# Kernel optimization log

Measured on AMD Instinct MI355X. Metric: run time of the kernel, lower is better.

Reference implementation:

```python
import jax, jax.numpy as jnp
import numpy as np

B, L, DM, H, PD = 2, 1024, 512, 8, 64
D = DM // H  # head_dim = 64
NEG = -10000.0


def setup_inputs() -> dict:
    key = jax.random.key(0)
    ks = jax.random.split(key, 12)
    s = 1.0 / np.sqrt(DM)
    sp = 1.0 / np.sqrt(PD)
    return {
        "x": jax.random.normal(ks[0], (B, L, DM), dtype=jnp.float32),
        "z": jax.random.normal(ks[1], (B, L, L, PD), dtype=jnp.float32),
        "residue_mask": jnp.ones((B, L), dtype=bool),
        "Wq": jax.random.normal(ks[2], (DM, DM), dtype=jnp.float32) * s,
        "bq": jnp.zeros((DM,), dtype=jnp.float32),
        "Wk": jax.random.normal(ks[3], (DM, DM), dtype=jnp.float32) * s,
        "bk": jnp.zeros((DM,), dtype=jnp.float32),
        "Wv": jax.random.normal(ks[4], (DM, DM), dtype=jnp.float32) * s,
        "bv": jnp.zeros((DM,), dtype=jnp.float32),
        "Wo": jax.random.normal(ks[5], (DM, DM), dtype=jnp.float32) * s,
        "bo": jnp.zeros((DM,), dtype=jnp.float32),
        "Wpb": jax.random.normal(ks[6], (PD, H), dtype=jnp.float32) * sp,
    }


def reference(x, z, residue_mask, Wq, bq, Wk, bk, Wv, bv, Wo, bo, Wpb):
    b, l, c = x.shape
    scale = 1.0 / np.sqrt(D)
    # projections -> (B, H, L, D)
    q = (x @ Wq + bq).reshape(b, l, H, D).transpose(0, 2, 1, 3)
    k = (x @ Wk + bk).reshape(b, l, H, D).transpose(0, 2, 1, 3)
    v = (x @ Wv + bv).reshape(b, l, H, D).transpose(0, 2, 1, 3)
    # pair bias: (B, L, L, PD) @ (PD, H) -> (B, H, L, L)
    bias = jnp.einsum('bijp,ph->bhij', z, Wpb)
    logits = jnp.einsum('bhid,bhjd->bhij', q, k) * scale + bias
    key_ok = residue_mask[:, None, None, :]
    query_ok = residue_mask[:, None, :, None]
    logits = jnp.where(key_ok, logits, NEG)
    logits = jnp.where(query_ok, logits, NEG)
    attn = jax.nn.softmax(logits, axis=-1)
    out = jnp.einsum('bhij,bhjd->bhid', attn, v)
    out = out.transpose(0, 2, 1, 3).reshape(b, l, c)
    return out @ Wo + bo
```

## Files before the change

### kernel.cpp

```cpp
#include <hip/hip_runtime.h>

typedef __bf16 bf16;
typedef __attribute__((ext_vector_type(4))) __bf16 bf16x4;
typedef __attribute__((ext_vector_type(8))) __bf16 bf16x8;
typedef __attribute__((ext_vector_type(4))) float f32x4;
typedef __attribute__((ext_vector_type(4))) _Float16 f16x4;
typedef __attribute__((ext_vector_type(2))) _Float16 f16x2;

#define B_   2
#define L_   1024
#define DM_  512
#define H_   8
#define D_   64
#define PD_  64
#define NEG_VAL -10000.0f

#define XB_N   (2048*512)
#define WT_N   (1536*512)
#define WTO_N  (512*512)
#define WTPB_N (16*64)

static __device__ __forceinline__ f32x4 mfma_bf16(bf16x8 a, bf16x8 b, f32x4 c) {
  return __builtin_amdgcn_mfma_f32_16x16x32_bf16(a, b, c, 0, 0, 0);
}

__global__ __launch_bounds__(256) void prep_kernel(
    const float* __restrict__ x, const float* __restrict__ Wq, const float* __restrict__ Wk,
    const float* __restrict__ Wv, const float* __restrict__ Wo, const float* __restrict__ Wpb,
    bf16* __restrict__ xb, bf16* __restrict__ Wt, bf16* __restrict__ Wto, bf16* __restrict__ Wtpb) {
  const int total = XB_N + WT_N + WTO_N + WTPB_N;
  for (int idx = blockIdx.x * 256 + threadIdx.x; idx < total; idx += gridDim.x * 256) {
    if (idx < XB_N) {
      xb[idx] = (bf16)x[idx];
    } else if (idx < XB_N + WT_N) {
      int t = idx - XB_N;
      int n = t >> 9, kk = t & 511;
      int sel = n >> 9, nn = n & 511;
      const float* W = sel == 0 ? Wq : (sel == 1 ? Wk : Wv);
      Wt[t] = (bf16)W[kk * 512 + nn];
    } else if (idx < XB_N + WT_N + WTO_N) {
      int t = idx - XB_N - WT_N;
      int n = t >> 9, kk = t & 511;
      Wto[t] = (bf16)Wo[kk * 512 + n];
    } else {
      int t = idx - XB_N - WT_N - WTO_N;
      int n = t >> 6, kk = t & 63;
      Wtpb[t] = (n < 8) ? (bf16)Wpb[kk * 8 + n] : (bf16)0.0f;
    }
  }
}

__global__ __launch_bounds__(256) void qkv_gemm(
    const bf16* __restrict__ xb, const bf16* __restrict__ Wt,
    const float* __restrict__ bq, const float* __restrict__ bk, const float* __restrict__ bv,
    bf16* __restrict__ qb, bf16* __restrict__ kb, bf16* __restrict__ vT) {
  int wid = blockIdx.x * 4 + (threadIdx.x >> 6);
  int lane = threadIdx.x & 63;
  int mt = wid / 48, nt = wid - mt * 48;
  int row0 = mt * 32, col0 = nt * 32;
  int lr = lane & 15, lg = lane >> 4;
  const bf16* a0p = xb + (row0 + lr) * 512 + lg * 8;
  const bf16* a1p = a0p + 16 * 512;
  const bf16* b0p = Wt + (col0 + lr) * 512 + lg * 8;
  const bf16* b1p = b0p + 16 * 512;
  f32x4 acc00 = {0.f,0.f,0.f,0.f}, acc01 = acc00, acc10 = acc00, acc11 = acc00;
#pragma unroll
  for (int kk = 0; kk < 512; kk += 32) {
    bf16x8 a0 = *reinterpret_cast<const bf16x8*>(a0p + kk);
    bf16x8 a1 = *reinterpret_cast<const bf16x8*>(a1p + kk);
    bf16x8 b0 = *reinterpret_cast<const bf16x8*>(b0p + kk);
    bf16x8 b1 = *reinterpret_cast<const bf16x8*>(b1p + kk);
    acc00 = mfma_bf16(a0, b0, acc00);
    acc01 = mfma_bf16(a0, b1, acc01);
    acc10 = mfma_bf16(a1, b0, acc10);
    acc11 = mfma_bf16(a1, b1, acc11);
  }
#pragma unroll
  for (int ni = 0; ni < 2; ++ni) {
    int col = col0 + ni * 16 + lr;
    int wsel = col >> 9;
    int ncol = col & 511;
    int h = ncol >> 6, d = ncol & 63;
    const float* bias = wsel == 0 ? bq : (wsel == 1 ? bk : bv);
    float bval = bias[ncol];
#pragma unroll
    for (int mi = 0; mi < 2; ++mi) {
      f32x4 acc = (mi == 0) ? (ni == 0 ? acc00 : acc01) : (ni == 0 ? acc10 : acc11);
      int m0 = row0 + mi * 16 + lg * 4;
      int bidx = m0 >> 10, l0 = m0 & 1023;
      if (wsel == 2) {
        bf16x4 pv;
#pragma unroll
        for (int r = 0; r < 4; ++r) pv[r] = (bf16)(acc[r] + bval);
        *reinterpret_cast<bf16x4*>(vT + ((long)(bidx * H_ + h) * D_ + d) * L_ + l0) = pv;
      } else if (wsel == 0) {
#pragma unroll
        for (int r = 0; r < 4; ++r)
          qb[((long)(bidx * H_ + h) * L_ + l0 + r) * D_ + d] = (bf16)((acc[r] + bval) * 0.125f);
      } else {
#pragma unroll
        for (int r = 0; r < 4; ++r)
          kb[((long)(bidx * H_ + h) * L_ + l0 + r) * D_ + d] = (bf16)(acc[r] + bval);
      }
    }
  }
}

__global__ __launch_bounds__(256) void bias_gemm(
    const float* __restrict__ z, const bf16* __restrict__ Wtpb, _Float16* __restrict__ biasbuf) {
  __shared__ float zt_raw[64 * 64];
  __shared__ _Float16 bt[8][72];
  int tid = threadIdx.x;
  int w = tid >> 6, lane = tid & 63;
  int lr = lane & 15, lg = lane >> 4;
  char* zb = (char*)zt_raw;
  const char* zsrc = (const char*)(z + (long)blockIdx.x * 4096);
#pragma unroll
  for (int q = 0; q < 4; ++q) {
    int lb = q * 4096 + tid * 16;
    int row = lb >> 8, col = lb & 255;
    f32x4 v = *reinterpret_cast<const f32x4*>(zsrc + lb);
    *reinterpret_cast<f32x4*>(zb + row * 256 + (col ^ ((row & 7) << 5))) = v;
  }
  bf16x8 b0 = *reinterpret_cast<const bf16x8*>(Wtpb + lr * 64 + lg * 8);
  bf16x8 b1 = *reinterpret_cast<const bf16x8*>(Wtpb + lr * 64 + 32 + lg * 8);
  __syncthreads();
  int row = w * 16 + lr;
  int sw = (row & 7) << 5;
  const char* zr = zb + row * 256;
  f32x4 z0 = *reinterpret_cast<const f32x4*>(zr + ((lg * 32) ^ sw));
  f32x4 z1 = *reinterpret_cast<const f32x4*>(zr + (((lg * 32) ^ sw) + 16));
  f32x4 z2 = *reinterpret_cast<const f32x4*>(zr + ((128 + lg * 32) ^ sw));
  f32x4 z3 = *reinterpret_cast<const f32x4*>(zr + (((128 + lg * 32) ^ sw) + 16));
  bf16x8 a0, a1;
#pragma unroll
  for (int e = 0; e < 4; ++e) { a0[e] = (bf16)z0[e]; a0[e + 4] = (bf16)z1[e]; }
#pragma unroll
  for (int e = 0; e < 4; ++e) { a1[e] = (bf16)z2[e]; a1[e + 4] = (bf16)z3[e]; }
  f32x4 acc = {0.f, 0.f, 0.f, 0.f};
  acc = mfma_bf16(a0, b0, acc);
  acc = mfma_bf16(a1, b1, acc);
  __syncthreads();
  if (lr < 8) {
    f16x4 hv;
#pragma unroll
    for (int r = 0; r < 4; ++r) hv[r] = (_Float16)acc[r];
    *reinterpret_cast<f16x4*>(&bt[lr][w * 16 + lg * 4]) = hv;
  }
  __syncthreads();
  {
    int h = tid >> 5, part = tid & 31;
    long pb = (long)blockIdx.x * 64;
    int b = (int)(pb >> 20), i = ((int)(pb >> 10)) & 1023, j0 = (int)pb & 1023;
    _Float16* dst = biasbuf + ((((long)b * H_ + h) * L_ + i) << 10) + j0 + part * 2;
    *reinterpret_cast<f16x2*>(dst) = *reinterpret_cast<const f16x2*>(&bt[h][part * 2]);
  }
}

__global__ __launch_bounds__(256) void attn_kernel(
    const bf16* __restrict__ qb, const bf16* __restrict__ kb, const bf16* __restrict__ vT,
    const _Float16* __restrict__ biasbuf, const int* __restrict__ mask, bf16* __restrict__ attn_out) {
  __shared__ bf16  p_lds[4][16][64];
  __shared__ float o_lds[4][16][64];
  __shared__ float m_lds[4][16];
  __shared__ float l_lds[4][16];
  int bid = blockIdx.x;
  int b = bid >> 9, h = (bid >> 6) & 7, it = bid & 63;
  int i0 = it * 16;
  int tid = threadIdx.x, w = tid >> 6, lane = tid & 63, lr = lane & 15, lg = lane >> 4;

  const bf16* qrow = qb + ((long)(b * H_ + h) * L_ + i0 + lr) * D_ + lg * 8;
  bf16x8 qa0 = *reinterpret_cast<const bf16x8*>(qrow);
  bf16x8 qa1 = *reinterpret_cast<const bf16x8*>(qrow + 32);
  const bf16* kbase = kb + (long)(b * H_ + h) * L_ * D_;
  const bf16* vbase = vT + (long)(b * H_ + h) * D_ * L_;
  const _Float16* bias_base = biasbuf + ((long)(b * H_ + h) * L_ + i0) * L_;
  const int* mrow_mask = mask + b * L_;

  bool qok[4];
#pragma unroll
  for (int r = 0; r < 4; ++r) qok[r] = mrow_mask[i0 + lg * 4 + r] != 0;

  float mr[4] = {-3.0e38f, -3.0e38f, -3.0e38f, -3.0e38f};
  float lsum[4] = {0.f, 0.f, 0.f, 0.f};
  f32x4 o0 = {0.f,0.f,0.f,0.f}, o1 = o0, o2 = o0, o3 = o0;

  char* p_base = (char*)&p_lds[w][0][0];

  for (int jt = 0; jt < 4; ++jt) {
    int j0 = w * 256 + jt * 64;
    f32x4 s0, s1, s2, s3;
#pragma unroll
    for (int jsub = 0; jsub < 4; ++jsub) {
      int j = j0 + jsub * 16 + lr;
      f32x4 acc;
#pragma unroll
      for (int r = 0; r < 4; ++r) acc[r] = (float)bias_base[(long)(lg * 4 + r) * L_ + j];
      const bf16* kr = kbase + (long)j * D_ + lg * 8;
      acc = mfma_bf16(qa0, *reinterpret_cast<const bf16x8*>(kr), acc);
      acc = mfma_bf16(qa1, *reinterpret_cast<const bf16x8*>(kr + 32), acc);
      bool kok = mrow_mask[j] != 0;
      if (!kok) {
#pragma unroll
        for (int r = 0; r < 4; ++r) acc[r] = NEG_VAL;
      }
      if (jsub == 0) s0 = acc; else if (jsub == 1) s1 = acc; else if (jsub == 2) s2 = acc; else s3 = acc;
    }
#pragma unroll
    for (int r = 0; r < 4; ++r) {
      if (!qok[r]) { s0[r] = NEG_VAL; s1[r] = NEG_VAL; s2[r] = NEG_VAL; s3[r] = NEG_VAL; }
    }
#pragma unroll
    for (int r = 0; r < 4; ++r) {
      float mt_ = fmaxf(fmaxf(s0[r], s1[r]), fmaxf(s2[r], s3[r]));
#pragma unroll
      for (int off = 1; off <= 8; off <<= 1) mt_ = fmaxf(mt_, __shfl_xor(mt_, off));
      float mnew = fmaxf(mr[r], mt_);
      float alpha = __expf(mr[r] - mnew);
      mr[r] = mnew;
      float p0 = __expf(s0[r] - mnew);
      float p1 = __expf(s1[r] - mnew);
      float p2 = __expf(s2[r] - mnew);
      float p3 = __expf(s3[r] - mnew);
      float ps = p0 + p1 + p2 + p3;
#pragma unroll
      for (int off = 1; off <= 8; off <<= 1) ps += __shfl_xor(ps, off);
      lsum[r] = lsum[r] * alpha + ps;
      o0[r] *= alpha; o1[r] *= alpha; o2[r] *= alpha; o3[r] *= alpha;
      int row = lg * 4 + r;
      int sw = (row & 7) << 4;
      *(bf16*)(p_base + row * 128 + ((lr * 2) ^ sw)) = (bf16)p0;
      *(bf16*)(p_base + row * 128 + ((32 + lr * 2) ^ sw)) = (bf16)p1;
      *(bf16*)(p_base + row * 128 + ((64 + lr * 2) ^ sw)) = (bf16)p2;
      *(bf16*)(p_base + row * 128 + ((96 + lr * 2) ^ sw)) = (bf16)p3;
    }
    int swr = (lr & 7) << 4;
    bf16x8 pa0 = *(const bf16x8*)(p_base + lr * 128 + ((lg * 16) ^ swr));
    bf16x8 pa1 = *(const bf16x8*)(p_base + lr * 128 + ((64 + lg * 16) ^ swr));
#pragma unroll
    for (int dsub = 0; dsub < 4; ++dsub) {
      const bf16* vr = vbase + (long)(dsub * 16 + lr) * L_ + j0 + lg * 8;
      bf16x8 vb0 = *reinterpret_cast<const bf16x8*>(vr);
      bf16x8 vb1 = *reinterpret_cast<const bf16x8*>(vr + 32);
      f32x4 acc = (dsub == 0) ? o0 : (dsub == 1) ? o1 : (dsub == 2) ? o2 : o3;
      acc = mfma_bf16(pa0, vb0, acc);
      acc = mfma_bf16(pa1, vb1, acc);
      if (dsub == 0) o0 = acc; else if (dsub == 1) o1 = acc; else if (dsub == 2) o2 = acc; else o3 = acc;
    }
  }
#pragma unroll
  for (int r = 0; r < 4; ++r) {
    int row = lg * 4 + r;
    o_lds[w][row][0 * 16 + lr] = o0[r];
    o_lds[w][row][1 * 16 + lr] = o1[r];
    o_lds[w][row][2 * 16 + lr] = o2[r];
    o_lds[w][row][3 * 16 + lr] = o3[r];
    if (lr == 0) { m_lds[w][row] = mr[r]; l_lds[w][row] = lsum[r]; }
  }
  __syncthreads();
  {
    int row = tid >> 4, d0 = (tid & 15) * 4;
    float M = fmaxf(fmaxf(m_lds[0][row], m_lds[1][row]), fmaxf(m_lds[2][row], m_lds[3][row]));
    float lt = 0.f;
    float oacc[4] = {0.f, 0.f, 0.f, 0.f};
#pragma unroll
    for (int ww = 0; ww < 4; ++ww) {
      float c = __expf(m_lds[ww][row] - M);
      lt += c * l_lds[ww][row];
#pragma unroll
      for (int e = 0; e < 4; ++e) oacc[e] += c * o_lds[ww][row][d0 + e];
    }
    float inv = 1.0f / lt;
    bf16x4 ov;
#pragma unroll
    for (int e = 0; e < 4; ++e) ov[e] = (bf16)(oacc[e] * inv);
    *reinterpret_cast<bf16x4*>(attn_out + ((long)(b * L_ + i0 + row)) * DM_ + h * D_ + d0) = ov;
  }
}

__global__ __launch_bounds__(256) void out_gemm(
    const bf16* __restrict__ ab, const bf16* __restrict__ Wto,
    const float* __restrict__ bo, float* __restrict__ out) {
  int wid = blockIdx.x * 4 + (threadIdx.x >> 6);
  int lane = threadIdx.x & 63;
  int mt = wid >> 4, nt = wid & 15;
  int row0 = mt * 32, col0 = nt * 32;
  int lr = lane & 15, lg = lane >> 4;
  const bf16* a0p = ab + (row0 + lr) * 512 + lg * 8;
  const bf16* a1p = a0p + 16 * 512;
  const bf16* b0p = Wto + (col0 + lr) * 512 + lg * 8;
  const bf16* b1p = b0p + 16 * 512;
  f32x4 acc00 = {0.f,0.f,0.f,0.f}, acc01 = acc00, acc10 = acc00, acc11 = acc00;
#pragma unroll
  for (int kk = 0; kk < 512; kk += 32) {
    bf16x8 a0 = *reinterpret_cast<const bf16x8*>(a0p + kk);
    bf16x8 a1 = *reinterpret_cast<const bf16x8*>(a1p + kk);
    bf16x8 b0 = *reinterpret_cast<const bf16x8*>(b0p + kk);
    bf16x8 b1 = *reinterpret_cast<const bf16x8*>(b1p + kk);
    acc00 = mfma_bf16(a0, b0, acc00);
    acc01 = mfma_bf16(a0, b1, acc01);
    acc10 = mfma_bf16(a1, b0, acc10);
    acc11 = mfma_bf16(a1, b1, acc11);
  }
#pragma unroll
  for (int ni = 0; ni < 2; ++ni) {
    int col = col0 + ni * 16 + lr;
    float bval = bo[col];
#pragma unroll
    for (int mi = 0; mi < 2; ++mi) {
      f32x4 acc = (mi == 0) ? (ni == 0 ? acc00 : acc01) : (ni == 0 ? acc10 : acc11);
      int m0 = row0 + mi * 16 + lg * 4;
#pragma unroll
      for (int r = 0; r < 4; ++r) out[(long)(m0 + r) * 512 + col] = acc[r] + bval;
    }
  }
}

extern "C" void kernel_launch(void* const* d_in, const int* in_sizes, int n_in,
                              void* d_out, int out_size, void* d_ws, size_t ws_size,
                              hipStream_t stream) {
  const float* x    = (const float*)d_in[0];
  const float* z    = (const float*)d_in[1];
  const int*   mask = (const int*)d_in[2];
  const float* Wq   = (const float*)d_in[3];
  const float* bq   = (const float*)d_in[4];
  const float* Wk   = (const float*)d_in[5];
  const float* bk   = (const float*)d_in[6];
  const float* Wv   = (const float*)d_in[7];
  const float* bv   = (const float*)d_in[8];
  const float* Wo   = (const float*)d_in[9];
  const float* bo   = (const float*)d_in[10];
  const float* Wpb  = (const float*)d_in[11];

  char* ws = (char*)d_ws;
  bf16* xb        = (bf16*)(ws + 0);
  bf16* Wt        = (bf16*)(ws + 2097152);
  bf16* Wto       = (bf16*)(ws + 3670016);
  bf16* Wtpb      = (bf16*)(ws + 4194304);
  bf16* qbuf      = (bf16*)(ws + 4196352);
  bf16* kbuf      = (bf16*)(ws + 6293504);
  bf16* vTbuf     = (bf16*)(ws + 8390656);
  bf16* attn_out  = (bf16*)(ws + 10487808);
  _Float16* biasb = (_Float16*)(ws + 12584960);

  prep_kernel<<<2048, 256, 0, stream>>>(x, Wq, Wk, Wv, Wo, Wpb, xb, Wt, Wto, Wtpb);
  qkv_gemm<<<768, 256, 0, stream>>>(xb, Wt, bq, bk, bv, qbuf, kbuf, vTbuf);
  bias_gemm<<<32768, 256, 0, stream>>>(z, Wtpb, biasb);
  attn_kernel<<<1024, 256, 0, stream>>>(qbuf, kbuf, vTbuf, biasb, mask, attn_out);
  out_gemm<<<256, 256, 0, stream>>>(attn_out, Wto, bo, (float*)d_out);
}
```

Baseline: 194.6 us.

## Split attention keys across blocks with separate merge kernel; fold key mask into bias

The attention kernel is split into a partial kernel that processes half the keys per block (2048 blocks), writing per-wave partial O/m/l to global memory, followed by a merge8 kernel that combines 8 partials per row. The MFMA operands are swapped so each lane owns a query row, which turns the row reductions into two cross-lane shuffles and lets bias be loaded as vector f16x4. The key mask is applied in bias_gemm so it no longer has to be applied in the attention loop. The trade is extra global traffic for the partials and one more kernel launch.

New measurement: 202.2 us. 1.04x slower.

```diff
diff --git a/kernel.cpp b/kernel.cpp
--- a/kernel.cpp
+++ b/kernel.cpp
@@ -107,7 +107,8 @@
 }
 
 __global__ __launch_bounds__(256) void bias_gemm(
-    const float* __restrict__ z, const bf16* __restrict__ Wtpb, _Float16* __restrict__ biasbuf) {
+    const float* __restrict__ z, const bf16* __restrict__ Wtpb, const int* __restrict__ mask,
+    _Float16* __restrict__ biasbuf) {
   __shared__ float zt_raw[64 * 64];
   __shared__ _Float16 bt[8][72];
   int tid = threadIdx.x;
@@ -152,20 +153,22 @@
     int h = tid >> 5, part = tid & 31;
     long pb = (long)blockIdx.x * 64;
     int b = (int)(pb >> 20), i = ((int)(pb >> 10)) & 1023, j0 = (int)pb & 1023;
-    _Float16* dst = biasbuf + ((((long)b * H_ + h) * L_ + i) << 10) + j0 + part * 2;
-    *reinterpret_cast<f16x2*>(dst) = *reinterpret_cast<const f16x2*>(&bt[h][part * 2]);
-  }
-}
-
-__global__ __launch_bounds__(256) void attn_kernel(
+    int j = j0 + part * 2;
+    f16x2 v = *reinterpret_cast<const f16x2*>(&bt[h][part * 2]);
+    if (mask[b * L_ + j] == 0)     v[0] = (_Float16)NEG_VAL;
+    if (mask[b * L_ + j + 1] == 0) v[1] = (_Float16)NEG_VAL;
+    _Float16* dst = biasbuf + ((((long)b * H_ + h) * L_ + i) << 10) + j;
+    *reinterpret_cast<f16x2*>(dst) = v;
+  }
+}
+
+__global__ __launch_bounds__(256) void attn_part(
     const bf16* __restrict__ qb, const bf16* __restrict__ kb, const bf16* __restrict__ vT,
-    const _Float16* __restrict__ biasbuf, const int* __restrict__ mask, bf16* __restrict__ attn_out) {
-  __shared__ bf16  p_lds[4][16][64];
-  __shared__ float o_lds[4][16][64];
-  __shared__ float m_lds[4][16];
-  __shared__ float l_lds[4][16];
+    const _Float16* __restrict__ biasb, const int* __restrict__ mask,
+    float* __restrict__ part_o, float* __restrict__ part_m, float* __restrict__ part_l) {
+  __shared__ bf16 p_lds[4][16 * 64];
   int bid = blockIdx.x;
-  int b = bid >> 9, h = (bid >> 6) & 7, it = bid & 63;
+  int jc = bid & 1, it = (bid >> 1) & 63, h = (bid >> 7) & 7, b = bid >> 10;
   int i0 = it * 16;
   int tid = threadIdx.x, w = tid >> 6, lane = tid & 63, lr = lane & 15, lg = lane >> 4;
 
@@ -174,108 +177,116 @@
   bf16x8 qa1 = *reinterpret_cast<const bf16x8*>(qrow + 32);
   const bf16* kbase = kb + (long)(b * H_ + h) * L_ * D_;
   const bf16* vbase = vT + (long)(b * H_ + h) * D_ * L_;
-  const _Float16* bias_base = biasbuf + ((long)(b * H_ + h) * L_ + i0) * L_;
-  const int* mrow_mask = mask + b * L_;
-
-  bool qok[4];
-#pragma unroll
-  for (int r = 0; r < 4; ++r) qok[r] = mrow_mask[i0 + lg * 4 + r] != 0;
-
-  float mr[4] = {-3.0e38f, -3.0e38f, -3.0e38f, -3.0e38f};
-  float lsum[4] = {0.f, 0.f, 0.f, 0.f};
+  const _Float16* bias_base = biasb + ((long)(b * H_ + h) * L_ + i0) * L_;
+  bool qok = mask[b * L_ + i0 + lr] != 0;
+
+  float m = -3.0e38f, l = 0.f;
   f32x4 o0 = {0.f,0.f,0.f,0.f}, o1 = o0, o2 = o0, o3 = o0;
-
-  char* p_base = (char*)&p_lds[w][0][0];
-
-  for (int jt = 0; jt < 4; ++jt) {
-    int j0 = w * 256 + jt * 64;
+  char* pbuf = (char*)&p_lds[w][0];
+  int swz = (lr & 7) << 4;
+  int jbase = jc * 512 + w * 128;
+
+  for (int jt = 0; jt < 2; ++jt) {
+    int j0 = jbase + jt * 64;
     f32x4 s0, s1, s2, s3;
 #pragma unroll
-    for (int jsub = 0; jsub < 4; ++jsub) {
-      int j = j0 + jsub * 16 + lr;
+    for (int tile = 0; tile < 4; ++tile) {
+      f16x4 bv = *reinterpret_cast<const f16x4*>(bias_base + (long)lr * L_ + j0 + tile * 16 + lg * 4);
       f32x4 acc;
 #pragma unroll
-      for (int r = 0; r < 4; ++r) acc[r] = (float)bias_base[(long)(lg * 4 + r) * L_ + j];
-      const bf16* kr = kbase + (long)j * D_ + lg * 8;
-      acc = mfma_bf16(qa0, *reinterpret_cast<const bf16x8*>(kr), acc);
-      acc = mfma_bf16(qa1, *reinterpret_cast<const bf16x8*>(kr + 32), acc);
-      bool kok = mrow_mask[j] != 0;
-      if (!kok) {
-#pragma unroll
-        for (int r = 0; r < 4; ++r) acc[r] = NEG_VAL;
-      }
-      if (jsub == 0) s0 = acc; else if (jsub == 1) s1 = acc; else if (jsub == 2) s2 = acc; else s3 = acc;
-    }
+      for (int r = 0; r < 4; ++r) acc[r] = (float)bv[r];
+      const bf16* kr = kbase + (long)(j0 + tile * 16 + lr) * D_ + lg * 8;
+      acc = mfma_bf16(*reinterpret_cast<const bf16x8*>(kr), qa0, acc);
+      acc = mfma_bf16(*reinterpret_cast<const bf16x8*>(kr + 32), qa1, acc);
+      if (tile == 0) s0 = acc; else if (tile == 1) s1 = acc; else if (tile == 2) s2 = acc; else s3 = acc;
+    }
+    if (!qok) {
+#pragma unroll
+      for (int r = 0; r < 4; ++r) { s0[r] = NEG_VAL; s1[r] = NEG_VAL; s2[r] = NEG_VAL; s3[r] = NEG_VAL; }
+    }
+    float mt = s0[0];
+#pragma unroll
+    for (int r = 0; r < 4; ++r) mt = fmaxf(fmaxf(fmaxf(mt, s0[r]), fmaxf(s1[r], s2[r])), s3[r]);
+    mt = fmaxf(mt, __shfl_xor(mt, 16));
+    mt = fmaxf(mt, __shfl_xor(mt, 32));
+    float mnew = fmaxf(m, mt);
+    float alpha = __expf(m - mnew);
+    m = mnew;
+    f32x4 p0, p1, p2, p3;
+    float ps = 0.f;
 #pragma unroll
     for (int r = 0; r < 4; ++r) {
-      if (!qok[r]) { s0[r] = NEG_VAL; s1[r] = NEG_VAL; s2[r] = NEG_VAL; s3[r] = NEG_VAL; }
-    }
-#pragma unroll
-    for (int r = 0; r < 4; ++r) {
-      float mt_ = fmaxf(fmaxf(s0[r], s1[r]), fmaxf(s2[r], s3[r]));
-#pragma unroll
-      for (int off = 1; off <= 8; off <<= 1) mt_ = fmaxf(mt_, __shfl_xor(mt_, off));
-      float mnew = fmaxf(mr[r], mt_);
-      float alpha = __expf(mr[r] - mnew);
-      mr[r] = mnew;
-      float p0 = __expf(s0[r] - mnew);
-      float p1 = __expf(s1[r] - mnew);
-      float p2 = __expf(s2[r] - mnew);
-      float p3 = __expf(s3[r] - mnew);
-      float ps = p0 + p1 + p2 + p3;
-#pragma unroll
-      for (int off = 1; off <= 8; off <<= 1) ps += __shfl_xor(ps, off);
-      lsum[r] = lsum[r] * alpha + ps;
-      o0[r] *= alpha; o1[r] *= alpha; o2[r] *= alpha; o3[r] *= alpha;
-      int row = lg * 4 + r;
-      int sw = (row & 7) << 4;
-      *(bf16*)(p_base + row * 128 + ((lr * 2) ^ sw)) = (bf16)p0;
-      *(bf16*)(p_base + row * 128 + ((32 + lr * 2) ^ sw)) = (bf16)p1;
-      *(bf16*)(p_base + row * 128 + ((64 + lr * 2) ^ sw)) = (bf16)p2;
-      *(bf16*)(p_base + row * 128 + ((96 + lr * 2) ^ sw)) = (bf16)p3;
-    }
-    int swr = (lr & 7) << 4;
-    bf16x8 pa0 = *(const bf16x8*)(p_base + lr * 128 + ((lg * 16) ^ swr));
-    bf16x8 pa1 = *(const bf16x8*)(p_base + lr * 128 + ((64 + lg * 16) ^ swr));
-#pragma unroll
-    for (int dsub = 0; dsub < 4; ++dsub) {
-      const bf16* vr = vbase + (long)(dsub * 16 + lr) * L_ + j0 + lg * 8;
-      bf16x8 vb0 = *reinterpret_cast<const bf16x8*>(vr);
-      bf16x8 vb1 = *reinterpret_cast<const bf16x8*>(vr + 32);
-      f32x4 acc = (dsub == 0) ? o0 : (dsub == 1) ? o1 : (dsub == 2) ? o2 : o3;
-      acc = mfma_bf16(pa0, vb0, acc);
-      acc = mfma_bf16(pa1, vb1, acc);
-      if (dsub == 0) o0 = acc; else if (dsub == 1) o1 = acc; else if (dsub == 2) o2 = acc; else o3 = acc;
-    }
-  }
-#pragma unroll
-  for (int r = 0; r < 4; ++r) {
-    int row = lg * 4 + r;
-    o_lds[w][row][0 * 16 + lr] = o0[r];
-    o_lds[w][row][1 * 16 + lr] = o1[r];
-    o_lds[w][row][2 * 16 + lr] = o2[r];
-    o_lds[w][row][3 * 16 + lr] = o3[r];
-    if (lr == 0) { m_lds[w][row] = mr[r]; l_lds[w][row] = lsum[r]; }
-  }
-  __syncthreads();
-  {
-    int row = tid >> 4, d0 = (tid & 15) * 4;
-    float M = fmaxf(fmaxf(m_lds[0][row], m_lds[1][row]), fmaxf(m_lds[2][row], m_lds[3][row]));
-    float lt = 0.f;
-    float oacc[4] = {0.f, 0.f, 0.f, 0.f};
-#pragma unroll
-    for (int ww = 0; ww < 4; ++ww) {
-      float c = __expf(m_lds[ww][row] - M);
-      lt += c * l_lds[ww][row];
-#pragma unroll
-      for (int e = 0; e < 4; ++e) oacc[e] += c * o_lds[ww][row][d0 + e];
-    }
-    float inv = 1.0f / lt;
-    bf16x4 ov;
-#pragma unroll
-    for (int e = 0; e < 4; ++e) ov[e] = (bf16)(oacc[e] * inv);
-    *reinterpret_cast<bf16x4*>(attn_out + ((long)(b * L_ + i0 + row)) * DM_ + h * D_ + d0) = ov;
-  }
+      p0[r] = __expf(s0[r] - mnew); p1[r] = __expf(s1[r] - mnew);
+      p2[r] = __expf(s2[r] - mnew); p3[r] = __expf(s3[r] - mnew);
+      ps += p0[r] + p1[r] + p2[r] + p3[r];
+    }
+    ps += __shfl_xor(ps, 16);
+    ps += __shfl_xor(ps, 32);
+    l = l * alpha + ps;
+#pragma unroll
+    for (int r = 0; r < 4; ++r) { o0[r] *= alpha; o1[r] *= alpha; o2[r] *= alpha; o3[r] *= alpha; }
+#pragma unroll
+    for (int tile = 0; tile < 4; ++tile) {
+      f32x4 pv = (tile == 0) ? p0 : (tile == 1) ? p1 : (tile == 2) ? p2 : p3;
+      bf16x4 pb_;
+#pragma unroll
+      for (int r = 0; r < 4; ++r) pb_[r] = (bf16)pv[r];
+      *reinterpret_cast<bf16x4*>(pbuf + ((lr * 128 + tile * 32 + lg * 8) ^ swz)) = pb_;
+    }
+    bf16x8 pa0 = *reinterpret_cast<const bf16x8*>(pbuf + ((lr * 128 + lg * 16) ^ swz));
+    bf16x8 pa1 = *reinterpret_cast<const bf16x8*>(pbuf + ((lr * 128 + 64 + lg * 16) ^ swz));
+#pragma unroll
+    for (int dtile = 0; dtile < 4; ++dtile) {
+      const bf16* vr = vbase + (long)(dtile * 16 + lr) * L_ + j0 + lg * 8;
+      f32x4 acc = (dtile == 0) ? o0 : (dtile == 1) ? o1 : (dtile == 2) ? o2 : o3;
+      acc = mfma_bf16(*reinterpret_cast<const bf16x8*>(vr), pa0, acc);
+      acc = mfma_bf16(*reinterpret_cast<const bf16x8*>(vr + 32), pa1, acc);
+      if (dtile == 0) o0 = acc; else if (dtile == 1) o1 = acc; else if (dtile == 2) o2 = acc; else o3 = acc;
+    }
+  }
+  int wid = bid * 4 + w;
+  float* po = part_o + (long)wid * 1024;
+#pragma unroll
+  for (int dtile = 0; dtile < 4; ++dtile) {
+    f32x4 ov = (dtile == 0) ? o0 : (dtile == 1) ? o1 : (dtile == 2) ? o2 : o3;
+    *reinterpret_cast<f32x4*>(po + lr * 64 + dtile * 16 + lg * 4) = ov;
+  }
+  if (lg == 0) { part_m[wid * 16 + lr] = m; part_l[wid * 16 + lr] = l; }
+}
+
+__global__ __launch_bounds__(256) void merge8(
+    const float* __restrict__ part_o, const float* __restrict__ part_m,
+    const float* __restrict__ part_l, bf16* __restrict__ attn_out) {
+  int t = blockIdx.x * 256 + threadIdx.x;
+  int d0 = (t & 15) * 4;
+  int row = t >> 4;
+  int b = row >> 13, h = (row >> 10) & 7, i = row & 1023;
+  int it = i >> 4, il = i & 15;
+  int bid0 = ((b * H_ + h) * 64 + it) * 2;
+  float mv[8];
+  float M = -3.0e38f;
+#pragma unroll
+  for (int p = 0; p < 8; ++p) {
+    int wid = (bid0 + (p >> 2)) * 4 + (p & 3);
+    mv[p] = part_m[wid * 16 + il];
+    M = fmaxf(M, mv[p]);
+  }
+  float lt = 0.f;
+  float oa[4] = {0.f, 0.f, 0.f, 0.f};
+#pragma unroll
+  for (int p = 0; p < 8; ++p) {
+    int wid = (bid0 + (p >> 2)) * 4 + (p & 3);
+    float c = __expf(mv[p] - M);
+    lt += c * part_l[wid * 16 + il];
+    f32x4 ov = *reinterpret_cast<const f32x4*>(part_o + ((long)wid * 16 + il) * 64 + d0);
+#pragma unroll
+    for (int e = 0; e < 4; ++e) oa[e] += c * ov[e];
+  }
+  float inv = 1.0f / lt;
+  bf16x4 r_;
+#pragma unroll
+  for (int e = 0; e < 4; ++e) r_[e] = (bf16)(oa[e] * inv);
+  *reinterpret_cast<bf16x4*>(attn_out + ((long)(b * L_ + i)) * DM_ + h * D_ + d0) = r_;
 }
 
 __global__ __launch_bounds__(256) void out_gemm(
@@ -342,10 +353,14 @@
   bf16* vTbuf     = (bf16*)(ws + 8390656);
   bf16* attn_out  = (bf16*)(ws + 10487808);
   _Float16* biasb = (_Float16*)(ws + 12584960);
+  float* part_o   = (float*)(ws + 46139392);
+  float* part_m   = (float*)(ws + 79693824);
+  float* part_l   = (float*)(ws + 80218112);
 
   prep_kernel<<<2048, 256, 0, stream>>>(x, Wq, Wk, Wv, Wo, Wpb, xb, Wt, Wto, Wtpb);
   qkv_gemm<<<768, 256, 0, stream>>>(xb, Wt, bq, bk, bv, qbuf, kbuf, vTbuf);
-  bias_gemm<<<32768, 256, 0, stream>>>(z, Wtpb, biasb);
-  attn_kernel<<<1024, 256, 0, stream>>>(qbuf, kbuf, vTbuf, biasb, mask, attn_out);
+  bias_gemm<<<32768, 256, 0, stream>>>(z, Wtpb, mask, biasb);
+  attn_part<<<2048, 256, 0, stream>>>(qbuf, kbuf, vTbuf, biasb, mask, part_o, part_m, part_l);
+  merge8<<<1024, 256, 0, stream>>>(part_o, part_m, part_l, attn_out);
   out_gemm<<<256, 256, 0, stream>>>(attn_out, Wto, bo, (float*)d_out);
 }
```
